# Performance work log

Measured on AMD Instinct MI355X. Metric: run time of the kernel, lower is better.

## Reference

```python
import jax, jax.numpy as jnp
import numpy as np

Z_DIM = 2  # state dimension is hard-coded (fc1: Linear(2, H), fc3: Linear(H, 2))


def _mlp(z, W1, b1, W2, b2, W3, b3):
    # torch.nn.Linear: y = x @ W.T + b
    h = jax.nn.elu(z @ W1.T + b1)
    h = jax.nn.elu(h @ W2.T + b2)
    return h @ W3.T + b3


def setup_inputs() -> dict:
    key = jax.random.key(0)
    ks = jax.random.split(key, 8)
    B, H = 1_000_000, 64
    s_in = 1.0 / np.sqrt(Z_DIM)
    s_h = 1.0 / np.sqrt(H)
    u = lambda k, shp, s: jax.random.uniform(k, shp, jnp.float32, -s, s)
    return {
        "t": jax.random.normal(ks[0], (1,), jnp.float32),
        "z_and_logp": jax.random.normal(ks[1], (B, Z_DIM + 1), jnp.float32),
        "W1": u(ks[2], (H, Z_DIM), s_in),
        "b1": u(ks[3], (H,), s_in),
        "W2": u(ks[4], (H, H), s_h),
        "b2": u(ks[5], (H,), s_h),
        "W3": u(ks[6], (Z_DIM, H), s_h),
        "b3": u(ks[7], (Z_DIM,), s_h),
    }


def reference(t, z_and_logp, W1, b1, W2, b2, W3, b3):
    # t is an unused time argument (ODE solver interface).
    z = z_and_logp[:, :Z_DIM]  # [B, 2]; logp column is not used in forward
    f = lambda x: _mlp(x, W1, b1, W2, b2, W3, b3)

    # Exact Jacobian trace via forward-mode JVPs with unit tangents (Z_DIM=2,
    # so this small fixed loop mirrors the per-dim autograd loop in torch).
    dz_dt = None
    trace = jnp.zeros(z.shape[0], dtype=z.dtype)
    for i in range(Z_DIM):
        e = jnp.zeros_like(z).at[:, i].set(1.0)
        out, jz = jax.jvp(f, (z,), (e,))
        if dz_dt is None:
            dz_dt = out
        trace = trace + jz[:, i]

    dlogp_dt = -trace[:, None]  # [B, 1]
    return jnp.concatenate([dz_dt, dlogp_dt], axis=1)  # [B, 3]
```

## Files before the change

kernel.cpp:

```cpp
#include <hip/hip_runtime.h>
#include <hip/hip_bf16.h>


typedef short bf16x8 __attribute__((ext_vector_type(8)));
typedef float f32x4  __attribute__((ext_vector_type(4)));
typedef float f32x2  __attribute__((ext_vector_type(2)));
typedef int   i32x4  __attribute__((ext_vector_type(4)));

#define LO2(v) __builtin_shufflevector(v, v, 0, 1)
#define HI2(v) __builtin_shufflevector(v, v, 2, 3)

static __device__ __forceinline__ short f2bf(float x) {
    __hip_bfloat16 b = __float2bfloat16(x);
    return __builtin_bit_cast(short, b);
}

static __device__ __forceinline__ int cvt_pk_bf16(float lo, float hi) {
    int r;
    asm("v_cvt_pk_bf16_f32 %0, %1, %2" : "=v"(r) : "v"(lo), "v"(hi));
    return r;
}

__global__ __launch_bounds__(256) __attribute__((amdgpu_waves_per_eu(3, 3)))
void odefunc_mfma(const float* __restrict__ zin,
                  const float* __restrict__ W1, const float* __restrict__ b1,
                  const float* __restrict__ W2, const float* __restrict__ b2,
                  const float* __restrict__ W3, const float* __restrict__ b3,
                  float* __restrict__ out, int B, int ntiles)
{
    __shared__ f32x4 sC[96];

    const int lane = threadIdx.x & 63;
    const int quad = lane >> 4;
    const int col  = lane & 15;

    if (threadIdx.x < 64) {
        int i = threadIdx.x;
        float* s = (float*)sC;
        s[i]       = W1[2*i];
        s[64 + i]  = W1[2*i + 1];
        s[128 + i] = b1[i];
        s[192 + i] = b2[i];
        s[256 + i] = W3[i];
        s[320 + i] = W3[64 + i];
    }

    const int wid    = blockIdx.x * (blockDim.x >> 6) + (threadIdx.x >> 6);
    const int nwaves = gridDim.x * (blockDim.x >> 6);

    bf16x8 aW2[4][2], aG[4][2];
#pragma unroll
    for (int mt = 0; mt < 4; ++mt) {
        const int k = mt * 16 + col;
        const float ck = W3[k], dk = W3[64 + k];
#pragma unroll
        for (int jt = 0; jt < 2; ++jt) {
            const float* p = W2 + k * 64 + jt * 32 + quad * 8;
#pragma unroll
            for (int jj = 0; jj < 8; ++jj) {
                int j = jt * 32 + quad * 8 + jj;
                float w2 = p[jj];
                aW2[mt][jt][jj] = f2bf(w2);
                aG[mt][jt][jj]  = f2bf(w2 * fmaf(ck, W1[2*j], dk * W1[2*j+1]));
            }
        }
    }

    const float b30 = b3[0], b31 = b3[1];
    const f32x4 zero4 = {0.f, 0.f, 0.f, 0.f};
    const f32x2 zerop = {0.f, 0.f};
    const f32x2 m1p   = {-1.f, -1.f};
    const f32x2 l2e   = {1.442695040888963f, 1.442695040888963f};

    __syncthreads();

    const int lload = lane < 48 ? lane : 47;
    int t = wid;
    float zv = 0.f;
    if (t < ntiles) zv = zin[t * 48 + lload];

    int cofs = 0;
    for (; t < ntiles; t += nwaves) {
        asm volatile("" : "+v"(cofs));

        int tn = t + nwaves;
        int tc = tn < ntiles ? tn : t;
        float zvn = zin[tc * 48 + lload];

        float z0 = __shfl(zv, 3 * col);
        float z1 = __shfl(zv, 3 * col + 1);
        const f32x2 z0p = {z0, z0}, z1p = {z1, z1};

        bf16x8 Bh[2], Bex[2];
#pragma unroll
        for (int jt = 0; jt < 2; ++jt) {
            int j4 = cofs + jt * 8 + quad * 2;
            f32x4 w0a = sC[j4],      w0b = sC[j4 + 1];
            f32x4 w1a = sC[j4 + 16], w1b = sC[j4 + 17];
            f32x4 bba = sC[j4 + 32], bbb = sC[j4 + 33];
            i32x4 ph, pe;
#pragma unroll
            for (int p = 0; p < 4; ++p) {
                f32x2 w0p = (p == 0) ? LO2(w0a) : (p == 1) ? HI2(w0a)
                           : (p == 2) ? LO2(w0b) : HI2(w0b);
                f32x2 w1p = (p == 0) ? LO2(w1a) : (p == 1) ? HI2(w1a)
                           : (p == 2) ? LO2(w1b) : HI2(w1b);
                f32x2 bbp = (p == 0) ? LO2(bba) : (p == 1) ? HI2(bba)
                           : (p == 2) ? LO2(bbb) : HI2(bbb);
                f32x2 a  = __builtin_elementwise_fma(w0p, z0p,
                           __builtin_elementwise_fma(w1p, z1p, bbp));
                f32x2 am = __builtin_elementwise_min(a, zerop);
                f32x2 tt = am * l2e;
                f32x2 e  = { __builtin_amdgcn_exp2f(tt[0]),
                             __builtin_amdgcn_exp2f(tt[1]) };
                f32x2 em1 = e + m1p;
                f32x2 h  = __builtin_elementwise_max(a, em1);
                ph[p] = cvt_pk_bf16(h[0], h[1]);
                pe[p] = cvt_pk_bf16(e[0], e[1]);
            }
            Bh[jt]  = __builtin_bit_cast(bf16x8, ph);
            Bex[jt] = __builtin_bit_cast(bf16x8, pe);
        }

        f32x4 accH[4], accT[4];
#pragma unroll
        for (int mt = 0; mt < 4; ++mt) {
            f32x4 b2v = sC[cofs + 48 + mt * 4 + quad];
            accH[mt] = __builtin_amdgcn_mfma_f32_16x16x32_bf16(aW2[mt][0], Bh[0], b2v, 0, 0, 0);
            accH[mt] = __builtin_amdgcn_mfma_f32_16x16x32_bf16(aW2[mt][1], Bh[1], accH[mt], 0, 0, 0);
            accT[mt] = __builtin_amdgcn_mfma_f32_16x16x32_bf16(aG[mt][0], Bex[0], zero4, 0, 0, 0);
            accT[mt] = __builtin_amdgcn_mfma_f32_16x16x32_bf16(aG[mt][1], Bex[1], accT[mt], 0, 0, 0);
        }

        f32x2 o0p = zerop, o1p = zerop, trcp = zerop;
#pragma unroll
        for (int mt = 0; mt < 4; ++mt) {
            int k4 = cofs + 48 + mt * 4 + quad;
            f32x4 w30 = sC[k4 + 16];
            f32x4 w31 = sC[k4 + 32];
#pragma unroll
            for (int half = 0; half < 2; ++half) {
                f32x2 a2  = half ? HI2(accH[mt]) : LO2(accH[mt]);
                f32x2 at  = half ? HI2(accT[mt]) : LO2(accT[mt]);
                f32x2 w30p = half ? HI2(w30) : LO2(w30);
                f32x2 w31p = half ? HI2(w31) : LO2(w31);
                f32x2 am = __builtin_elementwise_min(a2, zerop);
                f32x2 tt = am * l2e;
                f32x2 e  = { __builtin_amdgcn_exp2f(tt[0]),
                             __builtin_amdgcn_exp2f(tt[1]) };
                f32x2 em1 = e + m1p;
                f32x2 hh = __builtin_elementwise_max(a2, em1);
                o0p  = __builtin_elementwise_fma(w30p, hh, o0p);
                o1p  = __builtin_elementwise_fma(w31p, hh, o1p);
                trcp = __builtin_elementwise_fma(e, at, trcp);
            }
        }
        float o0 = o0p[0] + o0p[1];
        float o1 = o1p[0] + o1p[1];
        float trc = trcp[0] + trcp[1];

        o0  += __shfl_xor(o0, 16);  o0  += __shfl_xor(o0, 32);
        o1  += __shfl_xor(o1, 16);  o1  += __shfl_xor(o1, 32);
        trc += __shfl_xor(trc, 16); trc += __shfl_xor(trc, 32);

        int row = t * 16 + col;
        if (lane < 16 && row < B) {
            out[3 * row + 0] = o0 + b30;
            out[3 * row + 1] = o1 + b31;
            out[3 * row + 2] = -trc;
        }

        zv = zvn;
    }
}

extern "C" void kernel_launch(void* const* d_in, const int* in_sizes, int n_in,
                              void* d_out, int out_size, void* d_ws, size_t ws_size,
                              hipStream_t stream) {
    const float* zin = (const float*)d_in[1];
    const float* W1  = (const float*)d_in[2];
    const float* b1  = (const float*)d_in[3];
    const float* W2  = (const float*)d_in[4];
    const float* b2  = (const float*)d_in[5];
    const float* W3  = (const float*)d_in[6];
    const float* b3  = (const float*)d_in[7];
    float* out = (float*)d_out;

    int B = in_sizes[1] / 3;
    int ntiles = (B + 15) / 16;
    int grid = 1536;
    odefunc_mfma<<<grid, 256, 0, stream>>>(zin, W1, b1, W2, b2, W3, b3,
                                           out, B, ntiles);
}
```

Before: 123.4 us.

## Process two row tiles per wave iteration to increase per-wave ILP

Each wave now handles a pair of 16-row tiles per loop iteration, interleaving their ELU, MFMA and reduction chains so independent work can hide MFMA and transcendental latency. The launch drops to 2 waves per EU and a grid of 1024 blocks to match the larger register footprint. Fewer resident waves means less latency hiding from occupancy, and register pressure could cause spills.

Result: no change. 122.5 us (-0.8%).

```diff
diff --git a/kernel.cpp b/kernel.cpp
--- a/kernel.cpp
+++ b/kernel.cpp
@@ -21,7 +21,7 @@
     return r;
 }
 
-__global__ __launch_bounds__(256) __attribute__((amdgpu_waves_per_eu(3, 3)))
+__global__ __launch_bounds__(256) __attribute__((amdgpu_waves_per_eu(2, 2)))
 void odefunc_mfma(const float* __restrict__ zin,
                   const float* __restrict__ W1, const float* __restrict__ b1,
                   const float* __restrict__ W2, const float* __restrict__ b2,
@@ -75,30 +75,37 @@
     __syncthreads();
 
     const int lload = lane < 48 ? lane : 47;
-    int t = wid;
-    float zv = 0.f;
-    if (t < ntiles) zv = zin[t * 48 + lload];
+    int tp = wid;
+    float zvA = 0.f, zvB = 0.f;
+    if (2 * tp < ntiles)     zvA = zin[(2 * tp) * 48 + lload];
+    if (2 * tp + 1 < ntiles) zvB = zin[(2 * tp + 1) * 48 + lload];
 
     int cofs = 0;
-    for (; t < ntiles; t += nwaves) {
+    for (; 2 * tp < ntiles; tp += nwaves) {
         asm volatile("" : "+v"(cofs));
 
-        int tn = t + nwaves;
-        int tc = tn < ntiles ? tn : t;
-        float zvn = zin[tc * 48 + lload];
-
-        float z0 = __shfl(zv, 3 * col);
-        float z1 = __shfl(zv, 3 * col + 1);
-        const f32x2 z0p = {z0, z0}, z1p = {z1, z1};
-
-        bf16x8 Bh[2], Bex[2];
+        const int tA = 2 * tp, tB = 2 * tp + 1;
+        const bool vB = tB < ntiles;
+
+        int tpn = tp + nwaves;
+        int tAn = 2 * tpn     < ntiles ? 2 * tpn     : 0;
+        int tBn = 2 * tpn + 1 < ntiles ? 2 * tpn + 1 : 0;
+        float zvAn = zin[tAn * 48 + lload];
+        float zvBn = zin[tBn * 48 + lload];
+
+        float z0A = __shfl(zvA, 3 * col), z1A = __shfl(zvA, 3 * col + 1);
+        float z0B = __shfl(zvB, 3 * col), z1B = __shfl(zvB, 3 * col + 1);
+        const f32x2 z0Ap = {z0A, z0A}, z1Ap = {z1A, z1A};
+        const f32x2 z0Bp = {z0B, z0B}, z1Bp = {z1B, z1B};
+
+        bf16x8 BhA[2], BexA[2], BhB[2], BexB[2];
 #pragma unroll
         for (int jt = 0; jt < 2; ++jt) {
             int j4 = cofs + jt * 8 + quad * 2;
             f32x4 w0a = sC[j4],      w0b = sC[j4 + 1];
             f32x4 w1a = sC[j4 + 16], w1b = sC[j4 + 17];
             f32x4 bba = sC[j4 + 32], bbb = sC[j4 + 33];
-            i32x4 ph, pe;
+            i32x4 phA, peA, phB, peB;
 #pragma unroll
             for (int p = 0; p < 4; ++p) {
                 f32x2 w0p = (p == 0) ? LO2(w0a) : (p == 1) ? HI2(w0a)
@@ -107,32 +114,46 @@
                            : (p == 2) ? LO2(w1b) : HI2(w1b);
                 f32x2 bbp = (p == 0) ? LO2(bba) : (p == 1) ? HI2(bba)
                            : (p == 2) ? LO2(bbb) : HI2(bbb);
-                f32x2 a  = __builtin_elementwise_fma(w0p, z0p,
-                           __builtin_elementwise_fma(w1p, z1p, bbp));
-                f32x2 am = __builtin_elementwise_min(a, zerop);
-                f32x2 tt = am * l2e;
-                f32x2 e  = { __builtin_amdgcn_exp2f(tt[0]),
-                             __builtin_amdgcn_exp2f(tt[1]) };
-                f32x2 em1 = e + m1p;
-                f32x2 h  = __builtin_elementwise_max(a, em1);
-                ph[p] = cvt_pk_bf16(h[0], h[1]);
-                pe[p] = cvt_pk_bf16(e[0], e[1]);
+                f32x2 aA  = __builtin_elementwise_fma(w0p, z0Ap,
+                            __builtin_elementwise_fma(w1p, z1Ap, bbp));
+                f32x2 tAm = __builtin_elementwise_min(aA, zerop) * l2e;
+                f32x2 eA  = { __builtin_amdgcn_exp2f(tAm[0]),
+                              __builtin_amdgcn_exp2f(tAm[1]) };
+                f32x2 hA  = __builtin_elementwise_max(aA, eA + m1p);
+                f32x2 aB  = __builtin_elementwise_fma(w0p, z0Bp,
+                            __builtin_elementwise_fma(w1p, z1Bp, bbp));
+                f32x2 tBm = __builtin_elementwise_min(aB, zerop) * l2e;
+                f32x2 eB  = { __builtin_amdgcn_exp2f(tBm[0]),
+                              __builtin_amdgcn_exp2f(tBm[1]) };
+                f32x2 hB  = __builtin_elementwise_max(aB, eB + m1p);
+
+                phA[p] = cvt_pk_bf16(hA[0], hA[1]);
+                peA[p] = cvt_pk_bf16(eA[0], eA[1]);
+                phB[p] = cvt_pk_bf16(hB[0], hB[1]);
+                peB[p] = cvt_pk_bf16(eB[0], eB[1]);
             }
-            Bh[jt]  = __builtin_bit_cast(bf16x8, ph);
-            Bex[jt] = __builtin_bit_cast(bf16x8, pe);
-        }
-
-        f32x4 accH[4], accT[4];
+            BhA[jt]  = __builtin_bit_cast(bf16x8, phA);
+            BexA[jt] = __builtin_bit_cast(bf16x8, peA);
+            BhB[jt]  = __builtin_bit_cast(bf16x8, phB);
+            BexB[jt] = __builtin_bit_cast(bf16x8, peB);
+        }
+
+        f32x4 aHA[4], aTA[4], aHB[4], aTB[4];
 #pragma unroll
         for (int mt = 0; mt < 4; ++mt) {
             f32x4 b2v = sC[cofs + 48 + mt * 4 + quad];
-            accH[mt] = __builtin_amdgcn_mfma_f32_16x16x32_bf16(aW2[mt][0], Bh[0], b2v, 0, 0, 0);
-            accH[mt] = __builtin_amdgcn_mfma_f32_16x16x32_bf16(aW2[mt][1], Bh[1], accH[mt], 0, 0, 0);
-            accT[mt] = __builtin_amdgcn_mfma_f32_16x16x32_bf16(aG[mt][0], Bex[0], zero4, 0, 0, 0);
-            accT[mt] = __builtin_amdgcn_mfma_f32_16x16x32_bf16(aG[mt][1], Bex[1], accT[mt], 0, 0, 0);
-        }
-
-        f32x2 o0p = zerop, o1p = zerop, trcp = zerop;
+            aHA[mt] = __builtin_amdgcn_mfma_f32_16x16x32_bf16(aW2[mt][0], BhA[0], b2v, 0, 0, 0);
+            aHA[mt] = __builtin_amdgcn_mfma_f32_16x16x32_bf16(aW2[mt][1], BhA[1], aHA[mt], 0, 0, 0);
+            aHB[mt] = __builtin_amdgcn_mfma_f32_16x16x32_bf16(aW2[mt][0], BhB[0], b2v, 0, 0, 0);
+            aHB[mt] = __builtin_amdgcn_mfma_f32_16x16x32_bf16(aW2[mt][1], BhB[1], aHB[mt], 0, 0, 0);
+            aTA[mt] = __builtin_amdgcn_mfma_f32_16x16x32_bf16(aG[mt][0], BexA[0], zero4, 0, 0, 0);
+            aTA[mt] = __builtin_amdgcn_mfma_f32_16x16x32_bf16(aG[mt][1], BexA[1], aTA[mt], 0, 0, 0);
+            aTB[mt] = __builtin_amdgcn_mfma_f32_16x16x32_bf16(aG[mt][0], BexB[0], zero4, 0, 0, 0);
+            aTB[mt] = __builtin_amdgcn_mfma_f32_16x16x32_bf16(aG[mt][1], BexB[1], aTB[mt], 0, 0, 0);
+        }
+
+        f32x2 o0A = zerop, o1A = zerop, trA = zerop;
+        f32x2 o0B = zerop, o1B = zerop, trB = zerop;
 #pragma unroll
         for (int mt = 0; mt < 4; ++mt) {
             int k4 = cofs + 48 + mt * 4 + quad;
@@ -140,37 +161,53 @@
             f32x4 w31 = sC[k4 + 32];
 #pragma unroll
             for (int half = 0; half < 2; ++half) {
-                f32x2 a2  = half ? HI2(accH[mt]) : LO2(accH[mt]);
-                f32x2 at  = half ? HI2(accT[mt]) : LO2(accT[mt]);
                 f32x2 w30p = half ? HI2(w30) : LO2(w30);
                 f32x2 w31p = half ? HI2(w31) : LO2(w31);
-                f32x2 am = __builtin_elementwise_min(a2, zerop);
-                f32x2 tt = am * l2e;
-                f32x2 e  = { __builtin_amdgcn_exp2f(tt[0]),
-                             __builtin_amdgcn_exp2f(tt[1]) };
-                f32x2 em1 = e + m1p;
-                f32x2 hh = __builtin_elementwise_max(a2, em1);
-                o0p  = __builtin_elementwise_fma(w30p, hh, o0p);
-                o1p  = __builtin_elementwise_fma(w31p, hh, o1p);
-                trcp = __builtin_elementwise_fma(e, at, trcp);
+                f32x2 a2A = half ? HI2(aHA[mt]) : LO2(aHA[mt]);
+                f32x2 atA = half ? HI2(aTA[mt]) : LO2(aTA[mt]);
+                f32x2 tmA = __builtin_elementwise_min(a2A, zerop) * l2e;
+                f32x2 e2A = { __builtin_amdgcn_exp2f(tmA[0]),
+                              __builtin_amdgcn_exp2f(tmA[1]) };
+                f32x2 hhA = __builtin_elementwise_max(a2A, e2A + m1p);
+                o0A = __builtin_elementwise_fma(w30p, hhA, o0A);
+                o1A = __builtin_elementwise_fma(w31p, hhA, o1A);
+                trA = __builtin_elementwise_fma(e2A, atA, trA);
+                f32x2 a2B = half ? HI2(aHB[mt]) : LO2(aHB[mt]);
+                f32x2 atB = half ? HI2(aTB[mt]) : LO2(aTB[mt]);
+                f32x2 tmB = __builtin_elementwise_min(a2B, zerop) * l2e;
+                f32x2 e2B = { __builtin_amdgcn_exp2f(tmB[0]),
+                              __builtin_amdgcn_exp2f(tmB[1]) };
+                f32x2 hhB = __builtin_elementwise_max(a2B, e2B + m1p);
+                o0B = __builtin_elementwise_fma(w30p, hhB, o0B);
+                o1B = __builtin_elementwise_fma(w31p, hhB, o1B);
+                trB = __builtin_elementwise_fma(e2B, atB, trB);
             }
         }
-        float o0 = o0p[0] + o0p[1];
-        float o1 = o1p[0] + o1p[1];
-        float trc = trcp[0] + trcp[1];
-
-        o0  += __shfl_xor(o0, 16);  o0  += __shfl_xor(o0, 32);
-        o1  += __shfl_xor(o1, 16);  o1  += __shfl_xor(o1, 32);
-        trc += __shfl_xor(trc, 16); trc += __shfl_xor(trc, 32);
-
-        int row = t * 16 + col;
-        if (lane < 16 && row < B) {
-            out[3 * row + 0] = o0 + b30;
-            out[3 * row + 1] = o1 + b31;
-            out[3 * row + 2] = -trc;
-        }
-
-        zv = zvn;
+        float o0a = o0A[0] + o0A[1], o1a = o1A[0] + o1A[1], tra = trA[0] + trA[1];
+        float o0b = o0B[0] + o0B[1], o1b = o1B[0] + o1B[1], trb = trB[0] + trB[1];
+
+        o0a += __shfl_xor(o0a, 16); o0a += __shfl_xor(o0a, 32);
+        o1a += __shfl_xor(o1a, 16); o1a += __shfl_xor(o1a, 32);
+        tra += __shfl_xor(tra, 16); tra += __shfl_xor(tra, 32);
+        o0b += __shfl_xor(o0b, 16); o0b += __shfl_xor(o0b, 32);
+        o1b += __shfl_xor(o1b, 16); o1b += __shfl_xor(o1b, 32);
+        trb += __shfl_xor(trb, 16); trb += __shfl_xor(trb, 32);
+
+        int rowA = tA * 16 + col;
+        if (lane < 16 && rowA < B) {
+            out[3 * rowA + 0] = o0a + b30;
+            out[3 * rowA + 1] = o1a + b31;
+            out[3 * rowA + 2] = -tra;
+        }
+        int rowB = tB * 16 + col;
+        if (lane < 16 && vB && rowB < B) {
+            out[3 * rowB + 0] = o0b + b30;
+            out[3 * rowB + 1] = o1b + b31;
+            out[3 * rowB + 2] = -trb;
+        }
+
+        zvA = zvAn;
+        zvB = zvBn;
     }
 }
 
@@ -188,7 +225,7 @@
 
     int B = in_sizes[1] / 3;
     int ntiles = (B + 15) / 16;
-    int grid = 1536;
+    int grid = 1024;
     odefunc_mfma<<<grid, 256, 0, stream>>>(zin, W1, b1, W2, b2, W3, b3,
                                            out, B, ntiles);
 }
```
